# Kernel tuning notes

Hardware: AMD Instinct MI355X
Metric: run time of the kernel (lower is better)

The kernel has to match this reference:

```python
import jax, jax.numpy as jnp
import numpy as np

EPS = 1e-5  # BatchNorm eps (torch default)

def setup_inputs() -> dict:
    key = jax.random.key(0)
    ks = jax.random.split(key, 24)
    B, NX, NY, F = 8, 128, 128, 128
    dims = [2 * F, 512, 256, 128, 64]
    d = {
        'x': jax.random.normal(ks[0], (B, NX, F), dtype=jnp.float32),
        'y': jax.random.normal(ks[1], (B, NY, F), dtype=jnp.float32),
    }
    i = 2
    for li, (din, dout) in enumerate(zip(dims[:-1], dims[1:]), start=1):
        d[f'w{li}'] = jax.random.normal(ks[i], (dout, din), dtype=jnp.float32) * (1.0 / np.sqrt(din)); i += 1
        d[f'b{li}'] = jax.random.normal(ks[i], (dout,), dtype=jnp.float32) * 0.02; i += 1
        if li < 4:  # BatchNorm1d on hidden layers only (eval mode: running stats)
            d[f'g{li}'] = 1.0 + 0.1 * jax.random.normal(ks[i], (dout,), dtype=jnp.float32); i += 1
            d[f'be{li}'] = 0.1 * jax.random.normal(ks[i], (dout,), dtype=jnp.float32); i += 1
            d[f'm{li}'] = 0.1 * jax.random.normal(ks[i], (dout,), dtype=jnp.float32); i += 1
            d[f'v{li}'] = 0.5 + jax.random.uniform(ks[i], (dout,), dtype=jnp.float32); i += 1
    return d

def _bn(h, g, be, m, v):
    # BatchNorm1d in eval mode over the channel (last) axis
    return (h - m) * (g * jax.lax.rsqrt(v + EPS)) + be

def reference(x, y,
              w1, b1, g1, be1, m1, v1,
              w2, b2, g2, be2, m2, v2,
              w3, b3, g3, be3, m3, v3,
              w4, b4):
    F = x.shape[-1]
    # First Linear on cat([x_i, y_j]) == split-weight broadcast add: avoids the
    # (B,nx,ny,2F) pairwise concat the torch code materializes (same math).
    wx, wy = w1[:, :F], w1[:, F:]                      # (512,F) each
    hx = jnp.einsum('bif,hf->bih', x, wx)              # (B,nx,512)
    hy = jnp.einsum('bjf,hf->bjh', y, wy)              # (B,ny,512)
    h = hx[:, :, None, :] + hy[:, None, :, :] + b1     # (B,nx,ny,512)
    h = jax.nn.relu(_bn(h, g1, be1, m1, v1))           # dropout is identity in eval
    h = jax.nn.relu(_bn(jnp.einsum('bijh,oh->bijo', h, w2) + b2, g2, be2, m2, v2))
    h = jax.nn.relu(_bn(jnp.einsum('bijh,oh->bijo', h, w3) + b3, g3, be3, m3, v3))
    e = jnp.einsum('bijh,oh->bijo', h, w4) + b4        # (B,nx,ny,64) embeddings
    # PSD path: einsum('bijk,bilk->bijl', e, e).sum(-1)
    #         == sum_k e[b,i,j,k] * (sum_l e[b,i,l,k])  -- avoids (B,nx,ny,ny)
    s = e.sum(axis=2)                                  # (B,nx,64)
    kernel = jnp.einsum('bijk,bik->bij', e, s)         # (B,nx,ny)
    return kernel
```

## Files before the change

### kernel.cpp

```cpp
#include <hip/hip_runtime.h>

#define EPS 1e-5f

typedef _Float16 half8 __attribute__((ext_vector_type(8)));
typedef _Float16 half4 __attribute__((ext_vector_type(4)));
typedef float f32x16 __attribute__((ext_vector_type(16)));
typedef float f32x4v __attribute__((ext_vector_type(4)));


__global__ __launch_bounds__(256)
void pre_kernel(
    const float* __restrict__ x, const float* __restrict__ y,
    const float* __restrict__ w1, const float* __restrict__ b1,
    const float* __restrict__ g1, const float* __restrict__ be1,
    const float* __restrict__ m1, const float* __restrict__ v1,
    const float* __restrict__ w2, const float* __restrict__ b2,
    const float* __restrict__ g2, const float* __restrict__ be2,
    const float* __restrict__ m2, const float* __restrict__ v2,
    const float* __restrict__ w3, const float* __restrict__ b3,
    const float* __restrict__ g3, const float* __restrict__ be3,
    const float* __restrict__ m3, const float* __restrict__ v3,
    const float* __restrict__ w4,
    _Float16* __restrict__ hxh, _Float16* __restrict__ hyh,
    _Float16* __restrict__ w2h, _Float16* __restrict__ w3h,
    _Float16* __restrict__ w4h,
    float* __restrict__ b2f, float* __restrict__ b3f)
{
    const int t = threadIdx.x;

    if (blockIdx.x >= 256) {
        int tid = (blockIdx.x - 256) * 256 + t;
        const int nth = 64 * 256;
        for (int idx = tid; idx < 256 * 512; idx += nth) {
            int n = idx >> 9, k = idx & 511;
            float a = g2[n] * rsqrtf(v2[n] + EPS);
            int addr = ((n >> 5) * 32 + (k >> 4)) * 512 + ((k >> 3) & 1) * 256 + (n & 31) * 8 + (k & 7);
            w2h[addr] = (_Float16)(a * w2[idx]);
        }
        for (int idx = tid; idx < 128 * 256; idx += nth) {
            int n = idx >> 8, k = idx & 255;
            float a = g3[n] * rsqrtf(v3[n] + EPS);
            int addr = ((n >> 5) * 16 + (k >> 4)) * 512 + ((k >> 3) & 1) * 256 + (n & 31) * 8 + (k & 7);
            w3h[addr] = (_Float16)(a * w3[idx]);
        }
        for (int idx = tid; idx < 64 * 128; idx += nth) {
            int n = idx >> 7, k = idx & 127;
            int addr = ((n >> 5) * 8 + (k >> 4)) * 512 + ((k >> 3) & 1) * 256 + (n & 31) * 8 + (k & 7);
            w4h[addr] = (_Float16)w4[idx];
        }
        if (tid < 256) {
            float a = g2[tid] * rsqrtf(v2[tid] + EPS);
            b2f[tid] = a * b2[tid] + be2[tid] - m2[tid] * a;
        } else if (tid < 384) {
            int n = tid - 256;
            float a = g3[n] * rsqrtf(v3[n] + EPS);
            b3f[n] = a * b3[n] + be3[n] - m3[n] * a;
        }
        return;
    }

    const int rg = blockIdx.x & 31;
    const int ng = (blockIdx.x >> 5) & 3;
    const int which = blockIdx.x >> 7;

    constexpr int LDA = 136;
    __shared__ _Float16 sh[32 * 136 + 128 * 136] __attribute__((aligned(16)));
    _Float16* xa = sh;
    _Float16* wb = sh + 32 * 136;

    const int rowbase = rg * 32;
    const float* src = which ? y : x;

#pragma unroll
    for (int p = 0; p < 4; ++p) {
        int c = p * 256 + t;
        int r = c >> 5, fo = (c & 31) * 4;
        f32x4v v = *(const f32x4v*)(src + (size_t)(rowbase + r) * 128 + fo);
        half4 h; h[0] = (_Float16)v[0]; h[1] = (_Float16)v[1];
        h[2] = (_Float16)v[2]; h[3] = (_Float16)v[3];
        *(half4*)(xa + r * LDA + fo) = h;
    }
#pragma unroll
    for (int p = 0; p < 16; ++p) {
        int c = p * 256 + t;
        int n = c >> 5, fo = (c & 31) * 4;
        f32x4v v = *(const f32x4v*)(w1 + (size_t)(ng * 128 + n) * 256 + which * 128 + fo);
        half4 h; h[0] = (_Float16)v[0]; h[1] = (_Float16)v[1];
        h[2] = (_Float16)v[2]; h[3] = (_Float16)v[3];
        *(half4*)(wb + n * LDA + fo) = h;
    }
    __syncthreads();

    const int wid = t >> 6;
    const int l = t & 63;
    const int l31 = l & 31, lh = l >> 5;

    f32x16 acc = (f32x16)0.f;
#pragma unroll
    for (int kc = 0; kc < 8; ++kc) {
        half8 af = *(const half8*)(xa + l31 * LDA + kc * 16 + lh * 8);
        half8 bf = *(const half8*)(wb + (wid * 32 + l31) * LDA + kc * 16 + lh * 8);
        acc = __builtin_amdgcn_mfma_f32_32x32x16_f16(af, bf, acc, 0, 0, 0);
    }

    const int n = ng * 128 + wid * 32 + l31;
    float alpha = g1[n] * rsqrtf(v1[n] + EPS);
    if (which == 0) {
        float bias = alpha * b1[n] + be1[n] - m1[n] * alpha;
#pragma unroll
        for (int r = 0; r < 16; ++r) {
            int m = (r & 3) + 8 * (r >> 2) + 4 * lh;
            hxh[(size_t)(rowbase + m) * 512 + n] = (_Float16)(alpha * acc[r] + bias);
        }
    } else {
        const int ks = n >> 4, lhh = (n >> 3) & 1, c = n & 7;
#pragma unroll
        for (int r = 0; r < 16; ++r) {
            int m = (r & 3) + 8 * (r >> 2) + 4 * lh;
            int R = rowbase + m;
            int bb = R >> 7, j = R & 127;
            int addr = bb * 65536 + ((j >> 5) * 32 + ks) * 512 + lhh * 256 + (j & 31) * 8 + c;
            hyh[addr] = (_Float16)(alpha * acc[r]);
        }
    }
}

__global__ __launch_bounds__(512, 4)
void fused_kernel(
    const _Float16* __restrict__ hxh, const _Float16* __restrict__ hyh,
    const _Float16* __restrict__ w2h, const _Float16* __restrict__ w3h,
    const _Float16* __restrict__ w4h,
    const float* __restrict__ b2f, const float* __restrict__ b3f,
    const float* __restrict__ b4,
    float* __restrict__ out)
{
    constexpr int LD2 = 264;
    constexpr int LD3 = 136;
    constexpr int LDE = 68;

    __shared__ char smem[3584 + 67584] __attribute__((aligned(16)));
    _Float16* hxs = (_Float16*)smem;
    float* spart  = (float*)(smem + 1024);
    float* ss     = (float*)(smem + 3072);
    char* R1 = smem + 3584;
    _Float16* a2  = (_Float16*)R1;
    _Float16* a3  = (_Float16*)R1;
    float*    es  = (float*)R1;

    const int b = blockIdx.x >> 7;
    const int i = blockIdx.x & 127;
    const int t = threadIdx.x;
    const int wid = t >> 6;
    const int l   = t & 63;
    const int l31 = l & 31;
    const int lh  = l >> 5;

    if (t < 64)
        *(half8*)(hxs + t * 8) = *(const half8*)(hxh + (size_t)(b * 128 + i) * 512 + t * 8);
    __syncthreads();

    const int wm = wid >> 2, wn = wid & 3;

    f32x16 acc2[2][2];
#pragma unroll
    for (int mt = 0; mt < 2; ++mt)
#pragma unroll
        for (int nt = 0; nt < 2; ++nt) acc2[mt][nt] = (f32x16)0.f;

    const _Float16* paf0 = hyh + (size_t)b * 65536 + (wm * 2) * 32 * 512 + l * 8;
    const _Float16* paf1 = paf0 + 32 * 512;
    const _Float16* pbf0 = w2h + (wn * 2) * 32 * 512 + l * 8;
    const _Float16* pbf1 = pbf0 + 32 * 512;

    auto LD = [&](half8& A0, half8& A1, half8& B0, half8& B1, int ks) {
        A0 = *(const half8*)(paf0 + ks * 512);
        A1 = *(const half8*)(paf1 + ks * 512);
        B0 = *(const half8*)(pbf0 + ks * 512);
        B1 = *(const half8*)(pbf1 + ks * 512);
    };
    auto STEP = [&](half8 A0, half8 A1, half8 B0, half8 B1, int ks) {
        half8 rx = *(const half8*)(hxs + ks * 16 + lh * 8);
        half8 s0 = A0 + rx;
        half8 s1 = A1 + rx;
        half8 af0, af1;
#pragma unroll
        for (int c = 0; c < 8; ++c) {
            af0[c] = s0[c] > (_Float16)0.f ? s0[c] : (_Float16)0.f;
            af1[c] = s1[c] > (_Float16)0.f ? s1[c] : (_Float16)0.f;
        }
        acc2[0][0] = __builtin_amdgcn_mfma_f32_32x32x16_f16(af0, B0, acc2[0][0], 0, 0, 0);
        acc2[1][0] = __builtin_amdgcn_mfma_f32_32x32x16_f16(af1, B0, acc2[1][0], 0, 0, 0);
        acc2[0][1] = __builtin_amdgcn_mfma_f32_32x32x16_f16(af0, B1, acc2[0][1], 0, 0, 0);
        acc2[1][1] = __builtin_amdgcn_mfma_f32_32x32x16_f16(af1, B1, acc2[1][1], 0, 0, 0);
    };

    {
        half8 cA0, cA1, cB0, cB1, nA0, nA1, nB0, nB1;
        LD(cA0, cA1, cB0, cB1, 0);
#pragma unroll 2
        for (int ks = 0; ks < 32; ks += 2) {
            LD(nA0, nA1, nB0, nB1, ks + 1);
            STEP(cA0, cA1, cB0, cB1, ks);
            if (ks + 2 < 32) LD(cA0, cA1, cB0, cB1, ks + 2);
            STEP(nA0, nA1, nB0, nB1, ks + 1);
        }
    }

    {
        float bb0 = b2f[wn * 64 + l31];
        float bb1 = b2f[wn * 64 + 32 + l31];
#pragma unroll
        for (int mt = 0; mt < 2; ++mt)
#pragma unroll
            for (int r = 0; r < 16; ++r) {
                int m = wm * 64 + mt * 32 + (r & 3) + 8 * (r >> 2) + 4 * lh;
                a2[m * LD2 + wn * 64 + l31]      = (_Float16)fmaxf(acc2[mt][0][r] + bb0, 0.f);
                a2[m * LD2 + wn * 64 + 32 + l31] = (_Float16)fmaxf(acc2[mt][1][r] + bb1, 0.f);
            }
    }
    __syncthreads();

    f32x16 acc3[2];
    acc3[0] = (f32x16)0.f; acc3[1] = (f32x16)0.f;
#pragma unroll 8
    for (int kc = 0; kc < 16; ++kc) {
        half8 bfr = *(const half8*)(w3h + (wn * 16 + kc) * 512 + l * 8);
        half8 af0 = *(const half8*)(a2 + (wm * 64 + l31) * LD2 + kc * 16 + lh * 8);
        half8 af1 = *(const half8*)(a2 + (wm * 64 + 32 + l31) * LD2 + kc * 16 + lh * 8);
        acc3[0] = __builtin_amdgcn_mfma_f32_32x32x16_f16(af0, bfr, acc3[0], 0, 0, 0);
        acc3[1] = __builtin_amdgcn_mfma_f32_32x32x16_f16(af1, bfr, acc3[1], 0, 0, 0);
    }
    __syncthreads();
    {
        float b3v = b3f[wn * 32 + l31];
#pragma unroll
        for (int mt = 0; mt < 2; ++mt)
#pragma unroll
            for (int r = 0; r < 16; ++r) {
                int m = wm * 64 + mt * 32 + (r & 3) + 8 * (r >> 2) + 4 * lh;
                a3[m * LD3 + wn * 32 + l31] = (_Float16)fmaxf(acc3[mt][r] + b3v, 0.f);
            }
    }
    __syncthreads();

    const int wm4 = wid >> 1, wn4 = wid & 1;
    f32x16 acc4 = (f32x16)0.f;
#pragma unroll
    for (int kc = 0; kc < 8; ++kc) {
        half8 afr = *(const half8*)(a3 + (wm4 * 32 + l31) * LD3 + kc * 16 + lh * 8);
        half8 bfr = *(const half8*)(w4h + (wn4 * 8 + kc) * 512 + l * 8);
        acc4 = __builtin_amdgcn_mfma_f32_32x32x16_f16(afr, bfr, acc4, 0, 0, 0);
    }
    __syncthreads();
    {
        float b4v = b4[wn4 * 32 + l31];
#pragma unroll
        for (int r = 0; r < 16; ++r) {
            int m = wm4 * 32 + (r & 3) + 8 * (r >> 2) + 4 * lh;
            es[m * LDE + wn4 * 32 + l31] = acc4[r] + b4v;
        }
    }
    __syncthreads();

    {
        float sv = 0.f;
#pragma unroll
        for (int jj = 0; jj < 16; ++jj) sv += es[(wid + jj * 8) * LDE + l];
        spart[wid * 64 + l] = sv;
    }
    __syncthreads();
    if (t < 64) {
        float s2 = 0.f;
#pragma unroll
        for (int r = 0; r < 8; ++r) s2 += spart[r * 64 + t];
        ss[t] = s2;
    }
    __syncthreads();
    {
        const int j = t >> 2, q = t & 3;
        float p = 0.f;
#pragma unroll
        for (int c = 0; c < 16; ++c) {
            int k = q + 4 * c;
            p += es[j * LDE + k] * ss[k];
        }
        p += __shfl_xor(p, 1);
        p += __shfl_xor(p, 2);
        if (q == 0) out[(size_t)(b * 128 + i) * 128 + j] = p;
    }
}

extern "C" void kernel_launch(void* const* d_in, const int* in_sizes, int n_in,
                              void* d_out, int out_size, void* d_ws, size_t ws_size,
                              hipStream_t stream)
{
    (void)in_sizes; (void)n_in; (void)out_size; (void)ws_size;

    const float* x   = (const float*)d_in[0];
    const float* y   = (const float*)d_in[1];
    const float* w1  = (const float*)d_in[2];
    const float* b1  = (const float*)d_in[3];
    const float* g1  = (const float*)d_in[4];
    const float* be1 = (const float*)d_in[5];
    const float* m1  = (const float*)d_in[6];
    const float* v1  = (const float*)d_in[7];
    const float* w2  = (const float*)d_in[8];
    const float* b2  = (const float*)d_in[9];
    const float* g2  = (const float*)d_in[10];
    const float* be2 = (const float*)d_in[11];
    const float* m2  = (const float*)d_in[12];
    const float* v2  = (const float*)d_in[13];
    const float* w3  = (const float*)d_in[14];
    const float* b3  = (const float*)d_in[15];
    const float* g3  = (const float*)d_in[16];
    const float* be3 = (const float*)d_in[17];
    const float* m3  = (const float*)d_in[18];
    const float* v3  = (const float*)d_in[19];
    const float* w4  = (const float*)d_in[20];
    const float* b4  = (const float*)d_in[21];
    float* out = (float*)d_out;

    float* b2f = (float*)d_ws;
    float* b3f = b2f + 256;
    _Float16* w2h = (_Float16*)(b3f + 128);
    _Float16* w3h = w2h + 131072;
    _Float16* w4h = w3h + 32768;
    _Float16* hxh = w4h + 8192;
    _Float16* hyh = hxh + 524288;

    hipLaunchKernelGGL(pre_kernel, dim3(320), dim3(256), 0, stream,
                       x, y, w1, b1, g1, be1, m1, v1,
                       w2, b2, g2, be2, m2, v2,
                       w3, b3, g3, be3, m3, v3,
                       w4,
                       hxh, hyh, w2h, w3h, w4h, b2f, b3f);

    hipLaunchKernelGGL(fused_kernel, dim3(1024), dim3(512), 0, stream,
                       hxh, hyh, w2h, w3h, w4h, b2f, b3f, b4, out);
}
```

Measured before the change: 67.42 us.

## Retile layer-2 GEMM so each wave computes a 32x128 tile with single relu'd A fragment

Layer 2 of the per-row MLP is retiled from a 2x2 grid of 32x32 tiles per wave (64 rows by 64 columns) to one 32-row by 128-column strip per wave. Each wave now builds one relu'd A fragment (hx+hy) per k-step instead of two, which halves the redundant add/relu work on the A side and loads four B fragments instead of two. The loop is fully unrolled. The bias adds for layers 2-4 are folded into the accumulator initialisation, removing them from the epilogues. The cost is more W2 traffic per wave and possibly higher register pressure from four B fragments double-buffered.

```diff
diff --git a/kernel.cpp b/kernel.cpp
--- a/kernel.cpp
+++ b/kernel.cpp
@@ -159,69 +159,65 @@
         *(half8*)(hxs + t * 8) = *(const half8*)(hxh + (size_t)(b * 128 + i) * 512 + t * 8);
     __syncthreads();
 
+    const int wm2 = wid >> 1;
+    const int wn2 = wid & 1;
+
+    const _Float16* pa = hyh + (size_t)b * 65536 + (size_t)(wm2 * 32) * 512 + l * 8;
+    const _Float16* pb = w2h + (size_t)(wn2 * 4) * 32 * 512 + l * 8;
+
+    f32x16 acc2[4];
+#pragma unroll
+    for (int nt = 0; nt < 4; ++nt)
+        acc2[nt] = (f32x16)(b2f[wn2 * 128 + nt * 32 + l31]);
+
+    auto LDA_ = [&](half8& A, int ks) {
+        A = *(const half8*)(pa + ks * 512);
+    };
+    auto LDB_ = [&](half8 (&B)[4], int ks) {
+#pragma unroll
+        for (int nt = 0; nt < 4; ++nt)
+            B[nt] = *(const half8*)(pb + (size_t)(nt * 32 + ks) * 512);
+    };
+    auto STEP = [&](half8 A, half8 (&B)[4], int ks) {
+        half8 rx = *(const half8*)(hxs + ks * 16 + lh * 8);
+        half8 s = A + rx;
+        half8 af;
+#pragma unroll
+        for (int c = 0; c < 8; ++c)
+            af[c] = s[c] > (_Float16)0.f ? s[c] : (_Float16)0.f;
+#pragma unroll
+        for (int nt = 0; nt < 4; ++nt)
+            acc2[nt] = __builtin_amdgcn_mfma_f32_32x32x16_f16(af, B[nt], acc2[nt], 0, 0, 0);
+    };
+
+    {
+        half8 A0, A1, B0[4], B1[4];
+        LDA_(A0, 0); LDB_(B0, 0);
+#pragma unroll
+        for (int ks = 0; ks < 32; ks += 2) {
+            if (ks + 1 < 32) { LDA_(A1, ks + 1); LDB_(B1, ks + 1); }
+            STEP(A0, B0, ks);
+            if (ks + 2 < 32) { LDA_(A0, ks + 2); LDB_(B0, ks + 2); }
+            if (ks + 1 < 32) STEP(A1, B1, ks + 1);
+        }
+    }
+
+#pragma unroll
+    for (int nt = 0; nt < 4; ++nt)
+#pragma unroll
+        for (int r = 0; r < 16; ++r) {
+            int m = wm2 * 32 + (r & 3) + 8 * (r >> 2) + 4 * lh;
+            a2[m * LD2 + wn2 * 128 + nt * 32 + l31] = (_Float16)fmaxf(acc2[nt][r], 0.f);
+        }
+    __syncthreads();
+
     const int wm = wid >> 2, wn = wid & 3;
-
-    f32x16 acc2[2][2];
-#pragma unroll
-    for (int mt = 0; mt < 2; ++mt)
-#pragma unroll
-        for (int nt = 0; nt < 2; ++nt) acc2[mt][nt] = (f32x16)0.f;
-
-    const _Float16* paf0 = hyh + (size_t)b * 65536 + (wm * 2) * 32 * 512 + l * 8;
-    const _Float16* paf1 = paf0 + 32 * 512;
-    const _Float16* pbf0 = w2h + (wn * 2) * 32 * 512 + l * 8;
-    const _Float16* pbf1 = pbf0 + 32 * 512;
-
-    auto LD = [&](half8& A0, half8& A1, half8& B0, half8& B1, int ks) {
-        A0 = *(const half8*)(paf0 + ks * 512);
-        A1 = *(const half8*)(paf1 + ks * 512);
-        B0 = *(const half8*)(pbf0 + ks * 512);
-        B1 = *(const half8*)(pbf1 + ks * 512);
-    };
-    auto STEP = [&](half8 A0, half8 A1, half8 B0, half8 B1, int ks) {
-        half8 rx = *(const half8*)(hxs + ks * 16 + lh * 8);
-        half8 s0 = A0 + rx;
-        half8 s1 = A1 + rx;
-        half8 af0, af1;
-#pragma unroll
-        for (int c = 0; c < 8; ++c) {
-            af0[c] = s0[c] > (_Float16)0.f ? s0[c] : (_Float16)0.f;
-            af1[c] = s1[c] > (_Float16)0.f ? s1[c] : (_Float16)0.f;
-        }
-        acc2[0][0] = __builtin_amdgcn_mfma_f32_32x32x16_f16(af0, B0, acc2[0][0], 0, 0, 0);
-        acc2[1][0] = __builtin_amdgcn_mfma_f32_32x32x16_f16(af1, B0, acc2[1][0], 0, 0, 0);
-        acc2[0][1] = __builtin_amdgcn_mfma_f32_32x32x16_f16(af0, B1, acc2[0][1], 0, 0, 0);
-        acc2[1][1] = __builtin_amdgcn_mfma_f32_32x32x16_f16(af1, B1, acc2[1][1], 0, 0, 0);
-    };
-
+    f32x16 acc3[2];
     {
-        half8 cA0, cA1, cB0, cB1, nA0, nA1, nB0, nB1;
-        LD(cA0, cA1, cB0, cB1, 0);
-#pragma unroll 2
-        for (int ks = 0; ks < 32; ks += 2) {
-            LD(nA0, nA1, nB0, nB1, ks + 1);
-            STEP(cA0, cA1, cB0, cB1, ks);
-            if (ks + 2 < 32) LD(cA0, cA1, cB0, cB1, ks + 2);
-            STEP(nA0, nA1, nB0, nB1, ks + 1);
-        }
-    }
-
-    {
-        float bb0 = b2f[wn * 64 + l31];
-        float bb1 = b2f[wn * 64 + 32 + l31];
-#pragma unroll
-        for (int mt = 0; mt < 2; ++mt)
-#pragma unroll
-            for (int r = 0; r < 16; ++r) {
-                int m = wm * 64 + mt * 32 + (r & 3) + 8 * (r >> 2) + 4 * lh;
-                a2[m * LD2 + wn * 64 + l31]      = (_Float16)fmaxf(acc2[mt][0][r] + bb0, 0.f);
-                a2[m * LD2 + wn * 64 + 32 + l31] = (_Float16)fmaxf(acc2[mt][1][r] + bb1, 0.f);
-            }
-    }
-    __syncthreads();
-
-    f32x16 acc3[2];
-    acc3[0] = (f32x16)0.f; acc3[1] = (f32x16)0.f;
+        float b3v = b3f[wn * 32 + l31];
+        acc3[0] = (f32x16)b3v;
+        acc3[1] = (f32x16)b3v;
+    }
 #pragma unroll 8
     for (int kc = 0; kc < 16; ++kc) {
         half8 bfr = *(const half8*)(w3h + (wn * 16 + kc) * 512 + l * 8);
@@ -231,20 +227,17 @@
         acc3[1] = __builtin_amdgcn_mfma_f32_32x32x16_f16(af1, bfr, acc3[1], 0, 0, 0);
     }
     __syncthreads();
-    {
-        float b3v = b3f[wn * 32 + l31];
-#pragma unroll
-        for (int mt = 0; mt < 2; ++mt)
-#pragma unroll
-            for (int r = 0; r < 16; ++r) {
-                int m = wm * 64 + mt * 32 + (r & 3) + 8 * (r >> 2) + 4 * lh;
-                a3[m * LD3 + wn * 32 + l31] = (_Float16)fmaxf(acc3[mt][r] + b3v, 0.f);
-            }
-    }
+#pragma unroll
+    for (int mt = 0; mt < 2; ++mt)
+#pragma unroll
+        for (int r = 0; r < 16; ++r) {
+            int m = wm * 64 + mt * 32 + (r & 3) + 8 * (r >> 2) + 4 * lh;
+            a3[m * LD3 + wn * 32 + l31] = (_Float16)fmaxf(acc3[mt][r], 0.f);
+        }
     __syncthreads();
 
     const int wm4 = wid >> 1, wn4 = wid & 1;
-    f32x16 acc4 = (f32x16)0.f;
+    f32x16 acc4 = (f32x16)(b4[wn4 * 32 + l31]);
 #pragma unroll
     for (int kc = 0; kc < 8; ++kc) {
         half8 afr = *(const half8*)(a3 + (wm4 * 32 + l31) * LD3 + kc * 16 + lh * 8);
@@ -252,13 +245,10 @@
         acc4 = __builtin_amdgcn_mfma_f32_32x32x16_f16(afr, bfr, acc4, 0, 0, 0);
     }
     __syncthreads();
-    {
-        float b4v = b4[wn4 * 32 + l31];
-#pragma unroll
-        for (int r = 0; r < 16; ++r) {
-            int m = wm4 * 32 + (r & 3) + 8 * (r >> 2) + 4 * lh;
-            es[m * LDE + wn4 * 32 + l31] = acc4[r] + b4v;
-        }
+#pragma unroll
+    for (int r = 0; r < 16; ++r) {
+        int m = wm4 * 32 + (r & 3) + 8 * (r >> 2) + 4 * lh;
+        es[m * LDE + wn4 * 32 + l31] = acc4[r];
     }
     __syncthreads();
 
```

After: 194.3 us. +188.2%, slower.
